# Kernel optimization log

Measured on AMD Instinct MI355X. Metric: run time of the kernel, lower is better.

The kernel has to match this reference:

```python
import jax, jax.numpy as jnp
import numpy as np

IMG_W, IMG_H = 800, 800
OH, OW = 7, 7


def setup_inputs() -> dict:
    key = jax.random.key(0)
    k1, k2, k3 = jax.random.split(key, 3)
    feature_map = jax.random.normal(k1, (1, 256, 200, 200), dtype=jnp.float32)
    # boxes in image pixel coords, x1<=x2 and y1<=y2
    xs = jnp.sort(jax.random.uniform(k2, (1024, 2), dtype=jnp.float32) * (IMG_W - 1), axis=1)
    ys = jnp.sort(jax.random.uniform(k3, (1024, 2), dtype=jnp.float32) * (IMG_H - 1), axis=1)
    boxes = jnp.stack([xs[:, 0], ys[:, 0], xs[:, 1], ys[:, 1]], axis=1)
    return {"feature_map": feature_map, "boxes": boxes}


def reference(feature_map, boxes):
    # feature_map: [1, C, H, W]; boxes: [N, 4] (x1, y1, x2, y2) in image coords
    fm = feature_map[0]                      # [C, H, W]
    C, H, W = fm.shape
    scale = jnp.array([W / IMG_W, H / IMG_H, W / IMG_W, H / IMG_H], dtype=boxes.dtype)
    b = jnp.floor(boxes * scale).astype(jnp.int32)
    x1 = jnp.clip(b[:, 0], 0, W - 1)
    y1 = jnp.clip(b[:, 1], 0, H - 1)
    x2 = jnp.clip(b[:, 2] + 1, x1 + 1, W)    # exclusive end, clamped like torch slicing
    y2 = jnp.clip(b[:, 3] + 1, y1 + 1, H)
    rh = y2 - y1                             # [N]
    rw = x2 - x1
    # adaptive_avg_pool2d bin edges: start=floor(i*L/O), end=ceil((i+1)*L/O)
    i = jnp.arange(OH)
    j = jnp.arange(OW)
    rs = y1[:, None] + (i[None, :] * rh[:, None]) // OH                  # [N, OH]
    re = y1[:, None] + ((i[None, :] + 1) * rh[:, None] + OH - 1) // OH
    cs = x1[:, None] + (j[None, :] * rw[:, None]) // OW                  # [N, OW]
    ce = x1[:, None] + ((j[None, :] + 1) * rw[:, None] + OW - 1) // OW
    # integral image with zero row/col padding: ii[c, r, k] = sum fm[c, :r, :k]
    ii = jnp.pad(jnp.cumsum(jnp.cumsum(fm, axis=1), axis=2), ((0, 0), (1, 0), (1, 0)))

    def S(r, c):  # r: [N, OH], c: [N, OW] -> [N, C, OH, OW]
        return ii[:, r[:, :, None], c[:, None, :]].transpose(1, 0, 2, 3)

    total = S(re, ce) - S(rs, ce) - S(re, cs) + S(rs, cs)               # [N, C, OH, OW]
    area = ((re - rs)[:, :, None] * (ce - cs)[:, None, :]).astype(fm.dtype)  # [N, OH, OW]
    return total / area[:, None, :, :]
```

## Files before the change

### kernel.cpp

```cpp
#include <hip/hip_runtime.h>

#define C_CH  256
#define H_FM  200
#define W_FM  200
#define N_BOX 1024
#define OHp   7
#define OWp   7
#define NG    8
#define CG    32
#define WC    (W_FM * C_CH)
#define NCHUNK 25
#define CHROWS 8
#define GSTRIDE (H_FM * W_FM * CG)
#define HSTRIDE (W_FM * CG)


__global__ __launch_bounds__(256) void transpose_wscan_kernel(const float* __restrict__ fm,
                                                              float* __restrict__ T2) {
    __shared__ float tile[W_FM][CG + 1];
    __shared__ float tot[8][CG + 1];
    __shared__ float offE[8][CG + 1];
    const int t = threadIdx.x;
    const int h = blockIdx.x;
    const int g = blockIdx.y;
    const int c0 = g * CG;

    #pragma unroll
    for (int s = 0; s < 25; ++s) {
        int flat = s * 256 + t;
        int ci = flat / W_FM;
        int w  = flat - ci * W_FM;
        tile[w][ci] = fm[(size_t)(c0 + ci) * (H_FM * W_FM) + (size_t)h * W_FM + w];
    }
    __syncthreads();

    const int cg  = t & 31;
    const int chb = t >> 5;
    {
        float acc = 0.0f;
        #pragma unroll
        for (int s = 0; s < 25; ++s) {
            acc += tile[chb * 25 + s][cg];
            tile[chb * 25 + s][cg] = acc;
        }
        tot[chb][cg] = acc;
    }
    __syncthreads();

    {
        float off = 0.0f;
        #pragma unroll
        for (int k = 0; k < 8; ++k) {
            float v = tot[k][cg];
            if (k < chb) off += v;
        }
        offE[chb][cg] = off;
    }
    __syncthreads();

    float* dst = T2 + (size_t)g * GSTRIDE + (size_t)h * HSTRIDE;
    #pragma unroll
    for (int m = 0; m < 25; ++m) {
        int flat = m * 256 + t;
        int w  = flat >> 5;
        int cc = flat & 31;
        dst[flat] = tile[w][cc] + offE[w / 25][cc];
    }
}

__global__ __launch_bounds__(256) void colscan_chunk_kernel(float* __restrict__ T2,
                                                            float* __restrict__ aux) {
    const int col = blockIdx.x * 256 + threadIdx.x;
    const int ch  = blockIdx.y;
    const int g   = col / HSTRIDE;
    const int q   = col - g * HSTRIDE;
    float* p = T2 + (size_t)g * GSTRIDE + (size_t)(ch * CHROWS) * HSTRIDE + q;
    float acc = 0.0f;
    #pragma unroll
    for (int k = 0; k < CHROWS; ++k) {
        acc += p[(size_t)k * HSTRIDE];
        p[(size_t)k * HSTRIDE] = acc;
    }
    aux[(size_t)ch * WC + col] = acc;
}

__global__ __launch_bounds__(256) void aux_scan_kernel(float* __restrict__ aux) {
    const int col = blockIdx.x * 256 + threadIdx.x;
    float acc = 0.0f;
    #pragma unroll
    for (int ch = 0; ch < NCHUNK; ++ch) {
        float v = aux[(size_t)ch * WC + col];
        aux[(size_t)ch * WC + col] = acc;
        acc += v;
    }
}

__global__ __launch_bounds__(256) void add_offsets_kernel(float* __restrict__ T2,
                                                          const float* __restrict__ aux) {
    const int id = blockIdx.x * 256 + threadIdx.x;
    const int hh = id / (WC / 4);
    const int c4 = id - hh * (WC / 4);
    const int h  = hh + CHROWS;
    const int g  = c4 / (HSTRIDE / 4);
    const int q4 = c4 - g * (HSTRIDE / 4);
    const float4 o = ((const float4*)aux)[(size_t)(h >> 3) * (WC / 4) + c4];
    float4* tp = (float4*)T2 + (size_t)g * (GSTRIDE / 4) + (size_t)h * (HSTRIDE / 4) + q4;
    float4 v = *tp;
    v.x += o.x; v.y += o.y; v.z += o.z; v.w += o.w;
    *tp = v;
}

__global__ __launch_bounds__(256) void pool4_kernel(const float* __restrict__ T2,
                                                    const float* __restrict__ boxes,
                                                    float* __restrict__ out) {
    __shared__ float lo[CG * 49];
    const int bx = blockIdx.x;
    const int n  = bx >> 3;
    const int g  = bx & 7;
    const int t  = threadIdx.x;
    const int cg = t & 31;
    const int islot = t >> 5;

    const float4 box = ((const float4*)boxes)[n];
    int b0 = (int)floorf(box.x * 0.25f);
    int b1 = (int)floorf(box.y * 0.25f);
    int b2 = (int)floorf(box.z * 0.25f);
    int b3 = (int)floorf(box.w * 0.25f);
    int x1 = min(max(b0, 0), W_FM - 1);
    int y1 = min(max(b1, 0), H_FM - 1);
    int x2 = min(max(b2 + 1, x1 + 1), W_FM);
    int y2 = min(max(b3 + 1, y1 + 1), H_FM);
    int rh = y2 - y1;
    int rw = x2 - x1;

    if (islot < OHp) {
        const int i  = islot;
        const int rt = y1 + (i * rh) / OHp;
        const int rb = y1 + ((i + 1) * rh + OHp - 1) / OHp;
        int colv[2 * OWp];
        #pragma unroll
        for (int j = 0; j < OWp; ++j) {
            colv[j]       = x1 + (j * rw) / OWp;
            colv[OWp + j] = x1 + ((j + 1) * rw + OWp - 1) / OWp;
        }
        const float* base = T2 + (size_t)g * GSTRIDE + cg;
        const int ra = max(rt - 1, 0) * W_FM;
        const int rbm = (rb - 1) * W_FM;
        float top[2 * OWp], bot[2 * OWp];
        #pragma unroll
        for (int k = 0; k < 2 * OWp; ++k) {
            const int kk = colv[k];
            const int ka = max(kk - 1, 0);
            float tv = base[(size_t)(ra  + ka) * CG];
            float bv = base[(size_t)(rbm + ka) * CG];
            top[k] = (rt > 0 && kk > 0) ? tv : 0.0f;
            bot[k] = (kk > 0)           ? bv : 0.0f;
        }
        const float rowspan = (float)(rb - rt);
        #pragma unroll
        for (int j = 0; j < OWp; ++j) {
            float total = (bot[OWp + j] - bot[j]) - (top[OWp + j] - top[j]);
            float area  = rowspan * (float)(colv[OWp + j] - colv[j]);
            lo[cg * 49 + i * OWp + j] = total / area;
        }
    }
    __syncthreads();

    float* dst = out + (size_t)n * (C_CH * 49) + (size_t)g * (CG * 49);
    #pragma unroll
    for (int m = 0; m < 7; ++m) {
        int flat = m * 256 + t;
        if (flat < CG * 49) dst[flat] = lo[flat];
    }
}

__device__ __forceinline__ void box_edges(const float4 box, int i, int j,
                                          int& rs, int& re, int& cs, int& ce) {
    int b0 = (int)floorf(box.x * 0.25f);
    int b1 = (int)floorf(box.y * 0.25f);
    int b2 = (int)floorf(box.z * 0.25f);
    int b3 = (int)floorf(box.w * 0.25f);
    int x1 = min(max(b0, 0), W_FM - 1);
    int y1 = min(max(b1, 0), H_FM - 1);
    int x2 = min(max(b2 + 1, x1 + 1), W_FM);
    int y2 = min(max(b3 + 1, y1 + 1), H_FM);
    int rh = y2 - y1;
    int rw = x2 - x1;
    rs = y1 + (i * rh) / OHp;
    re = y1 + ((i + 1) * rh + OHp - 1) / OHp;
    cs = x1 + (j * rw) / OWp;
    ce = x1 + ((j + 1) * rw + OWp - 1) / OWp;
}

__global__ __launch_bounds__(256) void pool_direct_kernel(const float* __restrict__ fm,
                                                          const float* __restrict__ boxes,
                                                          float* __restrict__ out) {
    const int idx = blockIdx.x * 256 + threadIdx.x;
    const int j  = idx % OWp;
    const int t1 = idx / OWp;
    const int i  = t1 % OHp;
    const int t2 = t1 / OHp;
    const int c  = t2 % C_CH;
    const int n  = t2 / C_CH;

    const float4 box = ((const float4*)boxes)[n];
    int rs, re, cs, ce;
    box_edges(box, i, j, rs, re, cs, ce);

    const float* base = fm + (size_t)c * (H_FM * W_FM);
    float sum = 0.0f;
    for (int r = rs; r < re; ++r) {
        const float* rowp = base + (size_t)r * W_FM;
        for (int k = cs; k < ce; ++k) sum += rowp[k];
    }
    float area = (float)((re - rs) * (ce - cs));
    out[idx] = sum / area;
}

extern "C" void kernel_launch(void* const* d_in, const int* in_sizes, int n_in,
                              void* d_out, int out_size, void* d_ws, size_t ws_size,
                              hipStream_t stream) {
    const float* fm    = (const float*)d_in[0];
    const float* boxes = (const float*)d_in[1];
    float* out = (float*)d_out;

    const size_t tBytes   = (size_t)NG * GSTRIDE * sizeof(float);
    const size_t auxBytes = (size_t)NCHUNK * WC * sizeof(float);
    const int    total    = N_BOX * C_CH * OHp * OWp;
    const int    blocks   = total / 256;

    if (ws_size >= tBytes + auxBytes) {
        float* T2  = (float*)d_ws;
        float* aux = (float*)((char*)d_ws + tBytes);
        transpose_wscan_kernel<<<dim3(H_FM, NG), 256, 0, stream>>>(fm, T2);
        colscan_chunk_kernel<<<dim3(WC / 256, NCHUNK), 256, 0, stream>>>(T2, aux);
        aux_scan_kernel<<<WC / 256, 256, 0, stream>>>(aux);
        add_offsets_kernel<<<(H_FM - CHROWS) * (WC / 4) / 256, 256, 0, stream>>>(T2, aux);
        pool4_kernel<<<N_BOX * NG, 256, 0, stream>>>(T2, boxes, out);
    } else {
        pool_direct_kernel<<<blocks, 256, 0, stream>>>(fm, boxes, out);
    }
}
```

Baseline: 145.1 us.

## Drop add-offsets pass by folding chunk offsets into pooling lookups

Removes the add_offsets kernel that rewrote the whole integral image. The pooling kernel instead adds the per-chunk prefix offsets from a reorganised aux buffer at lookup time. The column-scan and aux-scan kernels now use float4 loads, and the output store is vectorised. This saves a full read-modify-write pass over the ~40MB table and one launch, at the cost of twice as many gather loads in pooling.

After: 141.4 us. 2.6% less time.

```diff
diff --git a/kernel.cpp b/kernel.cpp
--- a/kernel.cpp
+++ b/kernel.cpp
@@ -13,6 +13,7 @@
 #define CHROWS 8
 #define GSTRIDE (H_FM * W_FM * CG)
 #define HSTRIDE (W_FM * CG)
+#define AUXG    (NCHUNK * HSTRIDE)
 
 
 __global__ __launch_bounds__(256) void transpose_wscan_kernel(const float* __restrict__ fm,
@@ -69,51 +70,42 @@
 }
 
 __global__ __launch_bounds__(256) void colscan_chunk_kernel(float* __restrict__ T2,
-                                                            float* __restrict__ aux) {
-    const int col = blockIdx.x * 256 + threadIdx.x;
-    const int ch  = blockIdx.y;
-    const int g   = col / HSTRIDE;
-    const int q   = col - g * HSTRIDE;
-    float* p = T2 + (size_t)g * GSTRIDE + (size_t)(ch * CHROWS) * HSTRIDE + q;
-    float acc = 0.0f;
+                                                            float* __restrict__ aux2) {
+    const int q4 = blockIdx.x * 256 + threadIdx.x;
+    const int ch = blockIdx.y;
+    const int g  = q4 / (HSTRIDE / 4);
+    const int r4 = q4 - g * (HSTRIDE / 4);
+    float4* p = (float4*)T2 + (size_t)g * (GSTRIDE / 4)
+                            + (size_t)(ch * CHROWS) * (HSTRIDE / 4) + r4;
+    float4 acc = make_float4(0.f, 0.f, 0.f, 0.f);
     #pragma unroll
     for (int k = 0; k < CHROWS; ++k) {
-        acc += p[(size_t)k * HSTRIDE];
-        p[(size_t)k * HSTRIDE] = acc;
-    }
-    aux[(size_t)ch * WC + col] = acc;
-}
-
-__global__ __launch_bounds__(256) void aux_scan_kernel(float* __restrict__ aux) {
-    const int col = blockIdx.x * 256 + threadIdx.x;
-    float acc = 0.0f;
+        float4 v = p[(size_t)k * (HSTRIDE / 4)];
+        acc.x += v.x; acc.y += v.y; acc.z += v.z; acc.w += v.w;
+        p[(size_t)k * (HSTRIDE / 4)] = acc;
+    }
+    ((float4*)aux2)[(size_t)g * (AUXG / 4) + (size_t)ch * (HSTRIDE / 4) + r4] = acc;
+}
+
+__global__ __launch_bounds__(256) void aux_scan_kernel(float* __restrict__ aux2) {
+    const int idx = blockIdx.x * 256 + threadIdx.x;
+    const int g   = idx / (HSTRIDE / 4);
+    const int r4  = idx - g * (HSTRIDE / 4);
+    float4* p = (float4*)aux2 + (size_t)g * (AUXG / 4) + r4;
+    float4 acc = make_float4(0.f, 0.f, 0.f, 0.f);
     #pragma unroll
     for (int ch = 0; ch < NCHUNK; ++ch) {
-        float v = aux[(size_t)ch * WC + col];
-        aux[(size_t)ch * WC + col] = acc;
-        acc += v;
-    }
-}
-
-__global__ __launch_bounds__(256) void add_offsets_kernel(float* __restrict__ T2,
-                                                          const float* __restrict__ aux) {
-    const int id = blockIdx.x * 256 + threadIdx.x;
-    const int hh = id / (WC / 4);
-    const int c4 = id - hh * (WC / 4);
-    const int h  = hh + CHROWS;
-    const int g  = c4 / (HSTRIDE / 4);
-    const int q4 = c4 - g * (HSTRIDE / 4);
-    const float4 o = ((const float4*)aux)[(size_t)(h >> 3) * (WC / 4) + c4];
-    float4* tp = (float4*)T2 + (size_t)g * (GSTRIDE / 4) + (size_t)h * (HSTRIDE / 4) + q4;
-    float4 v = *tp;
-    v.x += o.x; v.y += o.y; v.z += o.z; v.w += o.w;
-    *tp = v;
-}
-
-__global__ __launch_bounds__(256) void pool4_kernel(const float* __restrict__ T2,
+        float4 v = p[(size_t)ch * (HSTRIDE / 4)];
+        p[(size_t)ch * (HSTRIDE / 4)] = acc;
+        acc.x += v.x; acc.y += v.y; acc.z += v.z; acc.w += v.w;
+    }
+}
+
+__global__ __launch_bounds__(256) void pool5_kernel(const float* __restrict__ T2,
+                                                    const float* __restrict__ aux2,
                                                     const float* __restrict__ boxes,
                                                     float* __restrict__ out) {
-    __shared__ float lo[CG * 49];
+    __shared__ __align__(16) float lo[CG * 49];
     const int bx = blockIdx.x;
     const int n  = bx >> 3;
     const int g  = bx & 7;
@@ -143,16 +135,19 @@
             colv[j]       = x1 + (j * rw) / OWp;
             colv[OWp + j] = x1 + ((j + 1) * rw + OWp - 1) / OWp;
         }
-        const float* base = T2 + (size_t)g * GSTRIDE + cg;
-        const int ra = max(rt - 1, 0) * W_FM;
+        const float* base = T2   + (size_t)g * GSTRIDE + cg;
+        const float* abase = aux2 + (size_t)g * AUXG   + cg;
+        const int ra  = max(rt - 1, 0) * W_FM;
         const int rbm = (rb - 1) * W_FM;
+        const int ca  = (max(rt - 1, 0) >> 3) * W_FM;
+        const int cb  = ((rb - 1) >> 3) * W_FM;
         float top[2 * OWp], bot[2 * OWp];
         #pragma unroll
         for (int k = 0; k < 2 * OWp; ++k) {
             const int kk = colv[k];
             const int ka = max(kk - 1, 0);
-            float tv = base[(size_t)(ra  + ka) * CG];
-            float bv = base[(size_t)(rbm + ka) * CG];
+            float tv = base[(size_t)(ra  + ka) * CG] + abase[(size_t)(ca + ka) * CG];
+            float bv = base[(size_t)(rbm + ka) * CG] + abase[(size_t)(cb + ka) * CG];
             top[k] = (rt > 0 && kk > 0) ? tv : 0.0f;
             bot[k] = (kk > 0)           ? bv : 0.0f;
         }
@@ -166,11 +161,12 @@
     }
     __syncthreads();
 
-    float* dst = out + (size_t)n * (C_CH * 49) + (size_t)g * (CG * 49);
-    #pragma unroll
-    for (int m = 0; m < 7; ++m) {
-        int flat = m * 256 + t;
-        if (flat < CG * 49) dst[flat] = lo[flat];
+    float4* dst4 = (float4*)(out + (size_t)n * (C_CH * 49) + (size_t)g * (CG * 49));
+    const float4* lo4 = (const float4*)lo;
+    #pragma unroll
+    for (int m = 0; m < 2; ++m) {
+        int idx = m * 256 + t;
+        if (idx < CG * 49 / 4) dst4[idx] = lo4[idx];
     }
 }
 
@@ -225,18 +221,17 @@
     float* out = (float*)d_out;
 
     const size_t tBytes   = (size_t)NG * GSTRIDE * sizeof(float);
-    const size_t auxBytes = (size_t)NCHUNK * WC * sizeof(float);
+    const size_t auxBytes = (size_t)NG * AUXG * sizeof(float);
     const int    total    = N_BOX * C_CH * OHp * OWp;
     const int    blocks   = total / 256;
 
     if (ws_size >= tBytes + auxBytes) {
-        float* T2  = (float*)d_ws;
-        float* aux = (float*)((char*)d_ws + tBytes);
+        float* T2   = (float*)d_ws;
+        float* aux2 = (float*)((char*)d_ws + tBytes);
         transpose_wscan_kernel<<<dim3(H_FM, NG), 256, 0, stream>>>(fm, T2);
-        colscan_chunk_kernel<<<dim3(WC / 256, NCHUNK), 256, 0, stream>>>(T2, aux);
-        aux_scan_kernel<<<WC / 256, 256, 0, stream>>>(aux);
-        add_offsets_kernel<<<(H_FM - CHROWS) * (WC / 4) / 256, 256, 0, stream>>>(T2, aux);
-        pool4_kernel<<<N_BOX * NG, 256, 0, stream>>>(T2, boxes, out);
+        colscan_chunk_kernel<<<dim3(WC / 4 / 256, NCHUNK), 256, 0, stream>>>(T2, aux2);
+        aux_scan_kernel<<<WC / 4 / 256, 256, 0, stream>>>(aux2);
+        pool5_kernel<<<N_BOX * NG, 256, 0, stream>>>(T2, aux2, boxes, out);
     } else {
         pool_direct_kernel<<<blocks, 256, 0, stream>>>(fm, boxes, out);
     }
```
